# Kernel optimization log

Hardware: AMD Instinct MI355X
Metric: run time of the kernel (lower is better)

Reference implementation:

```python
import jax, jax.numpy as jnp
import numpy as np

B, N, K, F, OUT = 32, 2000, 32, 64, 128

def setup_inputs() -> dict:
    key = jax.random.key(0)
    k1, k2, k3, k4, k5 = jax.random.split(key, 5)
    x = jax.random.normal(k1, (B, N, F), dtype=jnp.float32)
    neighborhood = jax.random.randint(k2, (N, K), 0, N, dtype=jnp.int64)
    distances = jax.random.uniform(k3, (N, K), dtype=jnp.float32)
    # Linear(k*(F+1), OUT): torch default init scale ~ 1/sqrt(fan_in)
    fan_in = K * (F + 1)
    W = jax.random.normal(k4, (OUT, fan_in), dtype=jnp.float32) / np.sqrt(fan_in)
    b = jax.random.normal(k5, (OUT,), dtype=jnp.float32) / np.sqrt(fan_in)
    return {"x": x, "neighborhood": neighborhood, "distances": distances, "W": W, "b": b}

def reference(x, neighborhood, distances, W, b):
    batch, seq_len, feat = x.shape          # [B, N, F]
    k = neighborhood.shape[1]
    gathered = x[:, neighborhood, :]        # [B, N, K, F] gather over sequence dim
    d = jnp.broadcast_to(distances[None, :, :, None], (batch, seq_len, k, 1))
    h = jnp.concatenate([gathered, d], axis=-1)        # [B, N, K, F+1]
    h = h.reshape(batch, seq_len, k * (feat + 1))      # [B, N, K*(F+1)]
    out = jnp.einsum('bnf,of->bno', h, W) + b          # [B, N, OUT]
    return out
```

## Files before the change

### kernel.cpp

```cpp
#include <hip/hip_runtime.h>
#include <hip/hip_bf16.h>
#include <stdint.h>

typedef __attribute__((ext_vector_type(8)))  __bf16   bf16x8;
typedef __attribute__((ext_vector_type(16))) float    f32x16;
typedef __attribute__((ext_vector_type(4)))  uint32_t u32x4;
typedef __attribute__((ext_vector_type(4)))  float    f32x4;

#define NB   32
#define NN   2000
#define NK   32
#define NF   64
#define NOUT 128
#define NSTEP 130

__global__ void kprep_x(const float* __restrict__ x, const float* __restrict__ dist,
                        __bf16* __restrict__ xb2, __bf16* __restrict__ db) {
  const int n = blockIdx.x;
  const int t = threadIdx.x;
  const int bb = t >> 3;
  const int f0 = (t & 7) << 3;
  const float* src = x + ((size_t)bb * NN + n) * NF + f0;
  f32x4 v0 = *(const f32x4*)(src);
  f32x4 v1 = *(const f32x4*)(src + 4);
  bf16x8 r;
  r[0] = (__bf16)v0[0]; r[1] = (__bf16)v0[1]; r[2] = (__bf16)v0[2]; r[3] = (__bf16)v0[3];
  r[4] = (__bf16)v1[0]; r[5] = (__bf16)v1[1]; r[6] = (__bf16)v1[2]; r[7] = (__bf16)v1[3];
  const int off = ((bb * 128) + (f0 << 1)) ^ ((bb & 7) << 4);
  *(bf16x8*)((char*)xb2 + ((size_t)n << 12) + off) = r;
  if (t < NK) db[n * NK + t] = (__bf16)dist[n * NK + t];
}

__global__ void kprep_w(const float* __restrict__ W, __bf16* __restrict__ Wf) {
  const int kstep = blockIdx.x;
  const int t = threadIdx.x;
  const int lane = t & 63;
  const int wv = t >> 6;
  const int o = wv * 32 + (lane & 31);
  const int kbase = kstep * 16 + (lane >> 5) * 8;
  bf16x8 r;
#pragma unroll
  for (int j = 0; j < 8; ++j) {
    const int kg = kbase + j;
    const int col = (kg < 2048) ? ((kg >> 6) * 65 + (kg & 63)) : ((kg - 2048) * 65 + 64);
    r[j] = (__bf16)W[(size_t)o * 2080 + col];
  }
  *(bf16x8*)(Wf + (((size_t)kstep * 256 + t) << 3)) = r;
}

__global__ __launch_bounds__(256, 4) void kmain(
    const int* __restrict__ nbrs, const float* __restrict__ bias,
    const __bf16* __restrict__ xb2, const __bf16* __restrict__ Wf,
    const __bf16* __restrict__ db, float* __restrict__ out) {
  __shared__ u32x4 lds[2][4][256];

  const int n0   = blockIdx.x * 2;
  const int t    = threadIdx.x;
  const int lane = t & 63;
  const int w    = t >> 6;
  const int col  = lane & 31;
  const int half = lane >> 5;
  const int swz  = col & 7;

  f32x16 acc0 = {};
  f32x16 acc1 = {};

  const __bf16* wfp = Wf + (((size_t)w * 64 + lane) << 3);

  for (int chunk = 0; chunk < 8; ++chunk) {
    u32x4 stg[8];
#pragma unroll
    for (int gg = 0; gg < 2; ++gg) {
#pragma unroll
      for (int c = 0; c < 4; ++c) {
        const int nb = nbrs[(n0 + gg) * NK + chunk * 4 + c];
        stg[gg * 4 + c] = *(const u32x4*)((const char*)xb2 + ((size_t)nb << 12) + t * 16);
      }
    }
    __syncthreads();
#pragma unroll
    for (int i = 0; i < 8; ++i) lds[i >> 2][i & 3][t] = stg[i];
    __syncthreads();

#pragma unroll
    for (int c = 0; c < 4; ++c) {
      const int sg = (chunk * 4 + c) * 4;
#pragma unroll
      for (int s = 0; s < 4; ++s) {
        bf16x8 bfr = *(const bf16x8*)(wfp + ((size_t)(sg + s) << 11));
        const int aoff = col * 8 + ((s * 2 + half) ^ swz);
        bf16x8 a0 = *(const bf16x8*)&lds[0][c][aoff];
        bf16x8 a1 = *(const bf16x8*)&lds[1][c][aoff];
        acc0 = __builtin_amdgcn_mfma_f32_32x32x16_bf16(a0, bfr, acc0, 0, 0, 0);
        acc1 = __builtin_amdgcn_mfma_f32_32x32x16_bf16(a1, bfr, acc1, 0, 0, 0);
      }
    }
  }

#pragma unroll
  for (int s = 0; s < 2; ++s) {
    bf16x8 bfr = *(const bf16x8*)(wfp + ((size_t)(128 + s) << 11));
    bf16x8 dv0 = *(const bf16x8*)((const char*)db + (size_t)n0 * 64 + s * 32 + half * 16);
    bf16x8 dv1 = *(const bf16x8*)((const char*)db + ((size_t)n0 + 1) * 64 + s * 32 + half * 16);
    acc0 = __builtin_amdgcn_mfma_f32_32x32x16_bf16(dv0, bfr, acc0, 0, 0, 0);
    acc1 = __builtin_amdgcn_mfma_f32_32x32x16_bf16(dv1, bfr, acc1, 0, 0, 0);
  }

  const int o = w * 32 + col;
  const float bv = bias[o];
#pragma unroll
  for (int r = 0; r < 16; ++r) {
    const int row = (r & 3) + 8 * (r >> 2) + 4 * half;
    out[((size_t)row * NN + n0) * NOUT + o]     = acc0[r] + bv;
    out[((size_t)row * NN + n0 + 1) * NOUT + o] = acc1[r] + bv;
  }
}

extern "C" void kernel_launch(void* const* d_in, const int* in_sizes, int n_in,
                              void* d_out, int out_size, void* d_ws, size_t ws_size,
                              hipStream_t stream) {
  const float* x    = (const float*)d_in[0];
  const int*   nbrs = (const int*)d_in[1];
  const float* dist = (const float*)d_in[2];
  const float* W    = (const float*)d_in[3];
  const float* bias = (const float*)d_in[4];
  float* out = (float*)d_out;

  char* ws = (char*)d_ws;
  __bf16* xb2 = (__bf16*)(ws);
  __bf16* Wf  = (__bf16*)(ws + 8192000);
  __bf16* db  = (__bf16*)(ws + 8192000 + 532480);

  kprep_x<<<NN, 256, 0, stream>>>(x, dist, xb2, db);
  kprep_w<<<NSTEP, 256, 0, stream>>>(W, Wf);
  kmain<<<NN / 2, 256, 0, stream>>>(nbrs, bias, xb2, Wf, db, out);
}
```

Baseline: 63.01 us.

## Double-buffer neighbor gathers with direct global-to-LDS loads

The main kernel now stages gathered neighbor rows straight into shared memory with global_load_lds instead of going through registers, and double-buffers LDS so the next chunk's gather overlaps the current chunk's MFMAs. Neighbor indices are loaded once per wave and broadcast with readlane, and the bf16 x layout is changed to a k-step-major layout so each lane reads a contiguous 16-byte fragment. This targets the gather latency and the register round-trip, at the cost of hand-written waitcnt and barrier ordering that must stay correct. The vmcnt(4) wait relies on the compiler not issuing other vector memory ops in between, such as the weight loads.

```diff
diff --git a/kernel.cpp b/kernel.cpp
--- a/kernel.cpp
+++ b/kernel.cpp
@@ -4,7 +4,6 @@
 
 typedef __attribute__((ext_vector_type(8)))  __bf16   bf16x8;
 typedef __attribute__((ext_vector_type(16))) float    f32x16;
-typedef __attribute__((ext_vector_type(4)))  uint32_t u32x4;
 typedef __attribute__((ext_vector_type(4)))  float    f32x4;
 
 #define NB   32
@@ -13,6 +12,9 @@
 #define NF   64
 #define NOUT 128
 #define NSTEP 130
+
+#define GLOBAL_AS __attribute__((address_space(1)))
+#define LDS_AS    __attribute__((address_space(3)))
 
 __global__ void kprep_x(const float* __restrict__ x, const float* __restrict__ dist,
                         __bf16* __restrict__ xb2, __bf16* __restrict__ db) {
@@ -26,7 +28,7 @@
   bf16x8 r;
   r[0] = (__bf16)v0[0]; r[1] = (__bf16)v0[1]; r[2] = (__bf16)v0[2]; r[3] = (__bf16)v0[3];
   r[4] = (__bf16)v1[0]; r[5] = (__bf16)v1[1]; r[6] = (__bf16)v1[2]; r[7] = (__bf16)v1[3];
-  const int off = ((bb * 128) + (f0 << 1)) ^ ((bb & 7) << 4);
+  const int off = ((f0 >> 4) << 10) + (((f0 >> 3) & 1) << 9) + (bb << 4);
   *(bf16x8*)((char*)xb2 + ((size_t)n << 12) + off) = r;
   if (t < NK) db[n * NK + t] = (__bf16)dist[n * NK + t];
 }
@@ -52,7 +54,7 @@
     const int* __restrict__ nbrs, const float* __restrict__ bias,
     const __bf16* __restrict__ xb2, const __bf16* __restrict__ Wf,
     const __bf16* __restrict__ db, float* __restrict__ out) {
-  __shared__ u32x4 lds[2][4][256];
+  __shared__ __align__(16) char lds[2][16384];
 
   const int n0   = blockIdx.x * 2;
   const int t    = threadIdx.x;
@@ -60,42 +62,58 @@
   const int w    = t >> 6;
   const int col  = lane & 31;
   const int half = lane >> 5;
-  const int swz  = col & 7;
+  const int g    = w >> 1;
+  const int c    = w & 1;
 
   f32x16 acc0 = {};
   f32x16 acc1 = {};
 
-  const __bf16* wfp = Wf + (((size_t)w * 64 + lane) << 3);
+  int myidx = 0;
+  if (lane < 16) myidx = nbrs[(n0 + g) * NK + lane * 2 + c];
 
-  for (int chunk = 0; chunk < 8; ++chunk) {
-    u32x4 stg[8];
+  const __bf16* wfp = Wf + (((size_t)(w * 64 + lane)) << 3);
+
+  auto stage = [&](int buf, int chunk) {
+    const int nb = __builtin_amdgcn_readlane(myidx, chunk);
+    const char* gsrc = (const char*)xb2 + ((size_t)nb << 12) + lane * 16;
+    char* ldst = &lds[buf][w << 12];
 #pragma unroll
-    for (int gg = 0; gg < 2; ++gg) {
+    for (int q = 0; q < 4; ++q) {
+      __builtin_amdgcn_global_load_lds(
+          (const GLOBAL_AS uint32_t*)(gsrc + (q << 10)),
+          (LDS_AS uint32_t*)(ldst + (q << 10)), 16, 0, 0);
+    }
+  };
+
+  auto compute = [&](int buf, int chunk) {
 #pragma unroll
-      for (int c = 0; c < 4; ++c) {
-        const int nb = nbrs[(n0 + gg) * NK + chunk * 4 + c];
-        stg[gg * 4 + c] = *(const u32x4*)((const char*)xb2 + ((size_t)nb << 12) + t * 16);
-      }
-    }
-    __syncthreads();
-#pragma unroll
-    for (int i = 0; i < 8; ++i) lds[i >> 2][i & 3][t] = stg[i];
-    __syncthreads();
-
-#pragma unroll
-    for (int c = 0; c < 4; ++c) {
-      const int sg = (chunk * 4 + c) * 4;
+    for (int cc = 0; cc < 2; ++cc) {
 #pragma unroll
       for (int s = 0; s < 4; ++s) {
-        bf16x8 bfr = *(const bf16x8*)(wfp + ((size_t)(sg + s) << 11));
-        const int aoff = col * 8 + ((s * 2 + half) ^ swz);
-        bf16x8 a0 = *(const bf16x8*)&lds[0][c][aoff];
-        bf16x8 a1 = *(const bf16x8*)&lds[1][c][aoff];
+        const int kstep = (chunk * 2 + cc) * 4 + s;
+        bf16x8 bfr = *(const bf16x8*)(wfp + ((size_t)kstep << 11));
+        bf16x8 a0 = *(const bf16x8*)&lds[buf][((0 * 2 + cc) << 12) + (s << 10) + lane * 16];
+        bf16x8 a1 = *(const bf16x8*)&lds[buf][((1 * 2 + cc) << 12) + (s << 10) + lane * 16];
         acc0 = __builtin_amdgcn_mfma_f32_32x32x16_bf16(a0, bfr, acc0, 0, 0, 0);
         acc1 = __builtin_amdgcn_mfma_f32_32x32x16_bf16(a1, bfr, acc1, 0, 0, 0);
       }
     }
+  };
+
+  stage(0, 0);
+  int cur = 0;
+  for (int chunk = 0; chunk < 15; ++chunk) {
+    stage(cur ^ 1, chunk + 1);
+    asm volatile("s_waitcnt vmcnt(4)" ::: "memory");
+    __builtin_amdgcn_s_barrier();
+    compute(cur, chunk);
+    asm volatile("s_waitcnt lgkmcnt(0)" ::: "memory");
+    __builtin_amdgcn_s_barrier();
+    cur ^= 1;
   }
+  asm volatile("s_waitcnt vmcnt(0)" ::: "memory");
+  __builtin_amdgcn_s_barrier();
+  compute(cur, 15);
 
 #pragma unroll
   for (int s = 0; s < 2; ++s) {
```

New measurement: 62.81 us. No clear change (-0.3%).

## Split K across two waves with direct global loads and LDS reduction

Applied to the files above, without the earlier changes.

Merges the two prep kernels into one launch, and the x prep now writes a layout that the MFMA A operand can read directly from global memory. The main kernel becomes 128-thread blocks in which each wave covers half of the K neighbours and all 128 outputs, keeping eight accumulators. Operands load straight from global/L2 with no LDS staging or barriers in the loop, and the two partial sums are combined through LDS at the end. This removes per-chunk syncs and staging traffic. In exchange it costs more registers, lower thread count per block, and repeated W reads with no LDS reuse.

```diff
diff --git a/kernel.cpp b/kernel.cpp
--- a/kernel.cpp
+++ b/kernel.cpp
@@ -4,115 +4,165 @@
 
 typedef __attribute__((ext_vector_type(8)))  __bf16   bf16x8;
 typedef __attribute__((ext_vector_type(16))) float    f32x16;
-typedef __attribute__((ext_vector_type(4)))  uint32_t u32x4;
 typedef __attribute__((ext_vector_type(4)))  float    f32x4;
+typedef __attribute__((ext_vector_type(8)))  float    f32x8;
 
-#define NB   32
 #define NN   2000
 #define NK   32
-#define NF   64
 #define NOUT 128
 #define NSTEP 130
 
-__global__ void kprep_x(const float* __restrict__ x, const float* __restrict__ dist,
-                        __bf16* __restrict__ xb2, __bf16* __restrict__ db) {
-  const int n = blockIdx.x;
+#define MFMA32 __builtin_amdgcn_mfma_f32_32x32x16_bf16
+
+__global__ void kprep(const float* __restrict__ x, const float* __restrict__ dist,
+                      const float* __restrict__ W,
+                      __bf16* __restrict__ xb2, __bf16* __restrict__ db,
+                      __bf16* __restrict__ Wf) {
   const int t = threadIdx.x;
-  const int bb = t >> 3;
-  const int f0 = (t & 7) << 3;
-  const float* src = x + ((size_t)bb * NN + n) * NF + f0;
-  f32x4 v0 = *(const f32x4*)(src);
-  f32x4 v1 = *(const f32x4*)(src + 4);
-  bf16x8 r;
-  r[0] = (__bf16)v0[0]; r[1] = (__bf16)v0[1]; r[2] = (__bf16)v0[2]; r[3] = (__bf16)v0[3];
-  r[4] = (__bf16)v1[0]; r[5] = (__bf16)v1[1]; r[6] = (__bf16)v1[2]; r[7] = (__bf16)v1[3];
-  const int off = ((bb * 128) + (f0 << 1)) ^ ((bb & 7) << 4);
-  *(bf16x8*)((char*)xb2 + ((size_t)n << 12) + off) = r;
-  if (t < NK) db[n * NK + t] = (__bf16)dist[n * NK + t];
+  if (blockIdx.x < NN) {
+    __shared__ __bf16 sm[32 * 66];
+    const int n = blockIdx.x;
+    const int bb = t >> 3;
+    const int f0 = (t & 7) << 3;
+    const float* src = x + ((size_t)bb * NN + n) * 64 + f0;
+    f32x8 v = *(const f32x8*)src;
+    bf16x8 r;
+#pragma unroll
+    for (int j = 0; j < 8; ++j) r[j] = (__bf16)v[j];
+    *(bf16x8*)&sm[bb * 66 + f0] = r;
+    __syncthreads();
+    const int col = t & 31, half = (t >> 5) & 1, s = t >> 6;
+    bf16x8 o = *(const bf16x8*)&sm[col * 66 + s * 16 + half * 8];
+    *(bf16x8*)((char*)xb2 + ((size_t)n << 12) + t * 16) = o;
+    if (t < NK) db[n * NK + t] = (__bf16)dist[n * NK + t];
+  } else {
+    const int kstep = blockIdx.x - NN;
+    const int lane = t & 63;
+    const int wv = t >> 6;
+    const int o = wv * 32 + (lane & 31);
+    const int kbase = kstep * 16 + (lane >> 5) * 8;
+    bf16x8 r;
+#pragma unroll
+    for (int j = 0; j < 8; ++j) {
+      const int kg = kbase + j;
+      const int c = (kg < 2048) ? ((kg >> 6) * 65 + (kg & 63)) : ((kg - 2048) * 65 + 64);
+      r[j] = (__bf16)W[(size_t)o * 2080 + c];
+    }
+    *(bf16x8*)(Wf + (((size_t)kstep * 256 + t) << 3)) = r;
+  }
 }
 
-__global__ void kprep_w(const float* __restrict__ W, __bf16* __restrict__ Wf) {
-  const int kstep = blockIdx.x;
-  const int t = threadIdx.x;
-  const int lane = t & 63;
-  const int wv = t >> 6;
-  const int o = wv * 32 + (lane & 31);
-  const int kbase = kstep * 16 + (lane >> 5) * 8;
-  bf16x8 r;
-#pragma unroll
-  for (int j = 0; j < 8; ++j) {
-    const int kg = kbase + j;
-    const int col = (kg < 2048) ? ((kg >> 6) * 65 + (kg & 63)) : ((kg - 2048) * 65 + 64);
-    r[j] = (__bf16)W[(size_t)o * 2080 + col];
-  }
-  *(bf16x8*)(Wf + (((size_t)kstep * 256 + t) << 3)) = r;
-}
-
-__global__ __launch_bounds__(256, 4) void kmain(
+__global__ __launch_bounds__(128) void kmain(
     const int* __restrict__ nbrs, const float* __restrict__ bias,
     const __bf16* __restrict__ xb2, const __bf16* __restrict__ Wf,
     const __bf16* __restrict__ db, float* __restrict__ out) {
-  __shared__ u32x4 lds[2][4][256];
+  __shared__ __align__(16) char red[32768];
 
-  const int n0   = blockIdx.x * 2;
   const int t    = threadIdx.x;
   const int lane = t & 63;
-  const int w    = t >> 6;
+  const int kh   = t >> 6;
   const int col  = lane & 31;
   const int half = lane >> 5;
-  const int swz  = col & 7;
+  const int n0   = blockIdx.x * 2;
 
-  f32x16 acc0 = {};
-  f32x16 acc1 = {};
+  f32x16 acc00 = {}, acc01 = {}, acc02 = {}, acc03 = {};
+  f32x16 acc10 = {}, acc11 = {}, acc12 = {}, acc13 = {};
 
-  const __bf16* wfp = Wf + (((size_t)w * 64 + lane) << 3);
+  int myidx = 0;
+  if ((lane & 31) < 16)
+    myidx = nbrs[(n0 + (lane >> 5)) * NK + kh * 16 + (lane & 15)];
 
-  for (int chunk = 0; chunk < 8; ++chunk) {
-    u32x4 stg[8];
+  const char* xb = (const char*)xb2;
+  const char* wf = (const char*)Wf + lane * 16;
+
+#pragma unroll 2
+  for (int cc = 0; cc < 16; ++cc) {
+    const int nbA = __builtin_amdgcn_readlane(myidx, cc);
+    const int nbB = __builtin_amdgcn_readlane(myidx, 32 + cc);
+    const char* gA = xb + ((size_t)nbA << 12) + lane * 16;
+    const char* gB = xb + ((size_t)nbB << 12) + lane * 16;
+    const char* wk = wf + ((size_t)((kh * 16 + cc) * 4) << 12);
 #pragma unroll
-    for (int gg = 0; gg < 2; ++gg) {
+    for (int ks = 0; ks < 4; ++ks) {
+      bf16x8 a0 = *(const bf16x8*)(gA + (ks << 10));
+      bf16x8 a1 = *(const bf16x8*)(gB + (ks << 10));
+      bf16x8 b0 = *(const bf16x8*)(wk + (ks << 12));
+      bf16x8 b1 = *(const bf16x8*)(wk + (ks << 12) + 1024);
+      bf16x8 b2 = *(const bf16x8*)(wk + (ks << 12) + 2048);
+      bf16x8 b3 = *(const bf16x8*)(wk + (ks << 12) + 3072);
+      acc00 = MFMA32(a0, b0, acc00, 0, 0, 0);
+      acc01 = MFMA32(a0, b1, acc01, 0, 0, 0);
+      acc02 = MFMA32(a0, b2, acc02, 0, 0, 0);
+      acc03 = MFMA32(a0, b3, acc03, 0, 0, 0);
+      acc10 = MFMA32(a1, b0, acc10, 0, 0, 0);
+      acc11 = MFMA32(a1, b1, acc11, 0, 0, 0);
+      acc12 = MFMA32(a1, b2, acc12, 0, 0, 0);
+      acc13 = MFMA32(a1, b3, acc13, 0, 0, 0);
+    }
+  }
+
+  if (kh == 0) {
 #pragma unroll
-      for (int c = 0; c < 4; ++c) {
-        const int nb = nbrs[(n0 + gg) * NK + chunk * 4 + c];
-        stg[gg * 4 + c] = *(const u32x4*)((const char*)xb2 + ((size_t)nb << 12) + t * 16);
-      }
+    for (int s = 0; s < 2; ++s) {
+      const char* wk = wf + ((size_t)(128 + s) << 12);
+      bf16x8 d0 = *(const bf16x8*)((const char*)db + (size_t)n0 * 64 + s * 32 + half * 16);
+      bf16x8 d1 = *(const bf16x8*)((const char*)db + (size_t)(n0 + 1) * 64 + s * 32 + half * 16);
+      bf16x8 b0 = *(const bf16x8*)(wk);
+      bf16x8 b1 = *(const bf16x8*)(wk + 1024);
+      bf16x8 b2 = *(const bf16x8*)(wk + 2048);
+      bf16x8 b3 = *(const bf16x8*)(wk + 3072);
+      acc00 = MFMA32(d0, b0, acc00, 0, 0, 0);
+      acc01 = MFMA32(d0, b1, acc01, 0, 0, 0);
+      acc02 = MFMA32(d0, b2, acc02, 0, 0, 0);
+      acc03 = MFMA32(d0, b3, acc03, 0, 0, 0);
+      acc10 = MFMA32(d1, b0, acc10, 0, 0, 0);
+      acc11 = MFMA32(d1, b1, acc11, 0, 0, 0);
+      acc12 = MFMA32(d1, b2, acc12, 0, 0, 0);
+      acc13 = MFMA32(d1, b3, acc13, 0, 0, 0);
     }
-    __syncthreads();
+  }
+
+  if (kh == 1) {
+    char* pb = red + lane * 64;
+    f32x16* a[8] = {&acc00,&acc01,&acc02,&acc03,&acc10,&acc11,&acc12,&acc13};
 #pragma unroll
-    for (int i = 0; i < 8; ++i) lds[i >> 2][i & 3][t] = stg[i];
-    __syncthreads();
-
+    for (int sl = 0; sl < 8; ++sl) {
 #pragma unroll
-    for (int c = 0; c < 4; ++c) {
-      const int sg = (chunk * 4 + c) * 4;
-#pragma unroll
-      for (int s = 0; s < 4; ++s) {
-        bf16x8 bfr = *(const bf16x8*)(wfp + ((size_t)(sg + s) << 11));
-        const int aoff = col * 8 + ((s * 2 + half) ^ swz);
-        bf16x8 a0 = *(const bf16x8*)&lds[0][c][aoff];
-        bf16x8 a1 = *(const bf16x8*)&lds[1][c][aoff];
-        acc0 = __builtin_amdgcn_mfma_f32_32x32x16_bf16(a0, bfr, acc0, 0, 0, 0);
-        acc1 = __builtin_amdgcn_mfma_f32_32x32x16_bf16(a1, bfr, acc1, 0, 0, 0);
+      for (int q = 0; q < 4; ++q) {
+        f32x4 v;
+        v[0] = (*a[sl])[q*4+0]; v[1] = (*a[sl])[q*4+1];
+        v[2] = (*a[sl])[q*4+2]; v[3] = (*a[sl])[q*4+3];
+        *(f32x4*)(pb + (sl << 12) + (q << 4)) = v;
       }
     }
   }
-
+  __syncthreads();
+  if (kh == 0) {
+    const char* pb = red + lane * 64;
+    f32x16* a[8] = {&acc00,&acc01,&acc02,&acc03,&acc10,&acc11,&acc12,&acc13};
 #pragma unroll
-  for (int s = 0; s < 2; ++s) {
-    bf16x8 bfr = *(const bf16x8*)(wfp + ((size_t)(128 + s) << 11));
-    bf16x8 dv0 = *(const bf16x8*)((const char*)db + (size_t)n0 * 64 + s * 32 + half * 16);
-    bf16x8 dv1 = *(const bf16x8*)((const char*)db + ((size_t)n0 + 1) * 64 + s * 32 + half * 16);
-    acc0 = __builtin_amdgcn_mfma_f32_32x32x16_bf16(dv0, bfr, acc0, 0, 0, 0);
-    acc1 = __builtin_amdgcn_mfma_f32_32x32x16_bf16(dv1, bfr, acc1, 0, 0, 0);
-  }
-
-  const int o = w * 32 + col;
-  const float bv = bias[o];
+    for (int sl = 0; sl < 8; ++sl) {
 #pragma unroll
-  for (int r = 0; r < 16; ++r) {
-    const int row = (r & 3) + 8 * (r >> 2) + 4 * half;
-    out[((size_t)row * NN + n0) * NOUT + o]     = acc0[r] + bv;
-    out[((size_t)row * NN + n0 + 1) * NOUT + o] = acc1[r] + bv;
+      for (int q = 0; q < 4; ++q) {
+        f32x4 v = *(const f32x4*)(pb + (sl << 12) + (q << 4));
+        (*a[sl])[q*4+0] += v[0]; (*a[sl])[q*4+1] += v[1];
+        (*a[sl])[q*4+2] += v[2]; (*a[sl])[q*4+3] += v[3];
+      }
+    }
+#pragma unroll
+    for (int og = 0; og < 4; ++og) {
+      const int o = og * 32 + col;
+      const float bv = bias[o];
+      const f32x16* c0 = (og==0)?&acc00:(og==1)?&acc01:(og==2)?&acc02:&acc03;
+      const f32x16* c1 = (og==0)?&acc10:(og==1)?&acc11:(og==2)?&acc12:&acc13;
+#pragma unroll
+      for (int r = 0; r < 16; ++r) {
+        const int row = (r & 3) + 8 * (r >> 2) + 4 * half;
+        float* op = out + ((size_t)row * NN + n0) * NOUT + o;
+        op[0]    = (*c0)[r] + bv;
+        op[NOUT] = (*c1)[r] + bv;
+      }
+    }
   }
 }
 
@@ -131,7 +181,6 @@
   __bf16* Wf  = (__bf16*)(ws + 8192000);
   __bf16* db  = (__bf16*)(ws + 8192000 + 532480);
 
-  kprep_x<<<NN, 256, 0, stream>>>(x, dist, xb2, db);
-  kprep_w<<<NSTEP, 256, 0, stream>>>(W, Wf);
-  kmain<<<NN / 2, 256, 0, stream>>>(nbrs, bias, xb2, Wf, db, out);
+  kprep<<<NN + NSTEP, 256, 0, stream>>>(x, dist, W, xb2, db, Wf);
+  kmain<<<NN / 2, 128, 0, stream>>>(nbrs, bias, xb2, Wf, db, out);
 }
```

New measurement: 79.36 us. 26.0% more time.
